# Performance work log

Measured on AMD Instinct MI355X. Metric: run time of the kernel, lower is better.

## Reference

```python
import jax, jax.numpy as jnp
import numpy as np

VOCAB, EMB, HDIM, VDIM, ATT = 30000, 256, 512, 128, 256
B, N, T = 64, 196, 32


def setup_inputs() -> dict:
    key = jax.random.key(0)
    ks = jax.random.split(key, 8)
    s = 0.02
    return {
        "V": jax.random.normal(ks[0], (B, N, VDIM), jnp.float32),
        "y": jax.random.randint(ks[1], (B, T), 0, VOCAB),
        "embed": jax.random.normal(ks[2], (VOCAB, EMB), jnp.float32) * s,
        "att_W_w": jax.random.normal(ks[3], (ATT, HDIM), jnp.float32) * s,
        "att_W_b": jnp.zeros((ATT,), jnp.float32),
        "att_U_w": jax.random.normal(ks[4], (ATT, VDIM), jnp.float32) * s,
        "att_U_b": jnp.zeros((ATT,), jnp.float32),
        "att_v_w": jax.random.normal(ks[5], (1, ATT), jnp.float32) * s,
        "att_v_b": jnp.zeros((1,), jnp.float32),
        "W_ih": jax.random.normal(ks[6], (4 * HDIM, EMB + VDIM), jnp.float32) * s,
        "W_hh": jax.random.normal(ks[7], (4 * HDIM, HDIM), jnp.float32) * s,
        "b_ih": jnp.zeros((4 * HDIM,), jnp.float32),
        "b_hh": jnp.zeros((4 * HDIM,), jnp.float32),
        "proj_w": jax.random.normal(jax.random.fold_in(key, 9), (EMB, HDIM), jnp.float32) * s,
    }


def reference(V, y, embed, att_W_w, att_W_b, att_U_w, att_U_b, att_v_w, att_v_b,
              W_ih, W_hh, b_ih, b_hh, proj_w):
    Bsz = y.shape[0]
    hdim = W_hh.shape[1]
    # loop-invariant U(V): [B, N, ATT]
    UV = jnp.einsum('bnv,av->bna', V, att_U_w) + att_U_b

    def step(carry, y_t):
        h, c, x_t = carry
        # additive attention
        Wh = h @ att_W_w.T + att_W_b                      # [B, ATT]
        e = jnp.tanh(Wh[:, None, :] + UV) @ att_v_w.T + att_v_b  # [B, N, 1]
        a = jax.nn.softmax(e, axis=1)
        ctx = jnp.sum(a * V, axis=1)                      # [B, VDIM]
        # LSTMCell (PyTorch gate order i, f, g, o)
        xc = jnp.concatenate([x_t, ctx], axis=-1)
        gates = xc @ W_ih.T + b_ih + h @ W_hh.T + b_hh
        i, f, g, o = jnp.split(gates, 4, axis=-1)
        c_new = jax.nn.sigmoid(f) * c + jax.nn.sigmoid(i) * jnp.tanh(g)
        h_new = jax.nn.sigmoid(o) * jnp.tanh(c_new)
        # dropout is identity in eval mode
        e_t = h_new @ proj_w.T                            # [B, EMB]
        logit = e_t @ embed.T                             # [B, VOCAB]
        x_next = embed[y_t]                               # teacher forcing
        return (h_new, c_new, x_next), logit

    h0 = jnp.zeros((Bsz, hdim), V.dtype)
    c0 = jnp.zeros((Bsz, hdim), V.dtype)
    x0 = embed[y[:, 0]]
    _, logits = jax.lax.scan(step, (h0, c0, x0), y[:, 1:].T)  # [T-1, B, VOCAB]
    return jnp.transpose(logits, (1, 0, 2))
```

## Files before the change

kernel.cpp:

```cpp
#include <hip/hip_runtime.h>
#include <stdint.h>

typedef unsigned short u16;
typedef uint32_t u32;
typedef short s16x8 __attribute__((ext_vector_type(8)));
typedef float f32x4 __attribute__((ext_vector_type(4)));

#define DEV __device__ __forceinline__

#define TSCALE 2.885390082f

DEV float bf2f(u16 h){ union{u32 u; float f;} x; x.u = ((u32)h)<<16; return x.f; }
DEV u16 f2bf(float f){ union{float f; u32 u;} x; x.f = f; u32 u = x.u;
  return (u16)((u + 0x7fffu + ((u>>16)&1u))>>16); }
DEV float bflo(u32 w){ union{u32 u; float f;} x; x.u = w<<16; return x.f; }
DEV float bfhi(u32 w){ union{u32 u; float f;} x; x.u = w & 0xffff0000u; return x.f; }

DEV float exp2_fast(float x){ return __builtin_amdgcn_exp2f(x); }
DEV float rcp_fast(float x){ return __builtin_amdgcn_rcpf(x); }
DEV float tanh2(float x){ float t = exp2_fast(TSCALE*x);
  return fmaf(-2.f, rcp_fast(t + 1.f), 1.f); }
DEV float sig2(float x){ return rcp_fast(1.f + exp2_fast(-1.442695041f*x)); }

DEV u32   ld_u(const u32* p){ return __hip_atomic_load(p, __ATOMIC_RELAXED, __HIP_MEMORY_SCOPE_AGENT); }
DEV void  st_u(u32* p, u32 v){ __hip_atomic_store(p, v, __ATOMIC_RELAXED, __HIP_MEMORY_SCOPE_AGENT); }

__global__ void f2b_kernel(const float* __restrict__ src, u16* __restrict__ dst, int n4, float scale){
  int i = blockIdx.x*blockDim.x + threadIdx.x;
  if (i < n4) {
    float4 v = ((const float4*)src)[i];
    ushort4 o; o.x = f2bf(v.x*scale); o.y = f2bf(v.y*scale); o.z = f2bf(v.z*scale); o.w = f2bf(v.w*scale);
    ((ushort4*)dst)[i] = o;
  }
}

__global__ void prep_wih2b(const float* __restrict__ Wih, u16* __restrict__ Wc){
  int idx = blockIdx.x*256 + threadIdx.x;
  int j = idx>>7, k = idx&127;
  Wc[idx] = f2bf(Wih[(size_t)j*384 + 256 + k]);
}

__global__ void repack_h(const u16* __restrict__ H2, u16* __restrict__ Hl){
  int r = blockIdx.x;
  int s = r>>6, b = r&63;
  int tid = threadIdx.x;
  u32 v = *((const u32*)(H2 + (size_t)(s+1)*32768 + (size_t)(tid>>2)*512 + (size_t)b*8) + (tid&3));
  ((u32*)(Hl + (size_t)r*512))[tid] = v;
}

__global__ __launch_bounds__(256) void gemm_bt(
    const u16* __restrict__ A, int lda,
    const u16* __restrict__ B, int ldb,
    const float* __restrict__ bias1, const float* __restrict__ bias2, float bscale,
    void* __restrict__ C, int ldc,
    int M, int N, int K, int Mt, int mode)
{
  __shared__ __align__(16) u16 As[64*64];
  __shared__ __align__(16) u16 Bs[128*64];
  int nwg = (int)gridDim.x;
  int b0 = blockIdx.x;
  int qq = nwg >> 3, rr = nwg & 7;
  int bswz;
  if (qq == 0) bswz = b0;
  else {
    int xcd = b0 & 7, i = b0 >> 3;
    bswz = (xcd < rr) ? (xcd*(qq+1) + i) : (rr*(qq+1) + (xcd - rr)*qq + i);
  }
  int mt = bswz % Mt, nt = bswz / Mt;
  int m0 = mt*64, n0 = nt*128;
  int tid = threadIdx.x, wave = tid>>6, lane = tid&63;
  int lrow = lane>>3, lcol = (lane&7)*8;
  f32x4 acc[2][4];
  #pragma unroll
  for (int i=0;i<2;i++)
    #pragma unroll
    for (int j=0;j<4;j++) acc[i][j] = (f32x4){0,0,0,0};
  int wm = (wave>>1)*32, wn = (wave&1)*64;
  int fr = lane&15, fk = (lane>>4)*8;
  for (int k0 = 0; k0 < K; k0 += 64) {
    __syncthreads();
    #pragma unroll
    for (int i = 0; i < 2; i++) {
      int ci = wave + i*4;
      int row = ci*8 + lrow;
      const u16* g = A + (size_t)(m0+row)*lda + k0 + lcol;
      __builtin_amdgcn_global_load_lds(
        (const __attribute__((address_space(1))) u32*)g,
        (__attribute__((address_space(3))) u32*)&As[ci*512], 16, 0, 0);
    }
    #pragma unroll
    for (int i = 0; i < 4; i++) {
      int ci = wave + i*4;
      int row = ci*8 + lrow;
      int gr = n0 + row; gr = gr < N ? gr : N-1;
      const u16* g = B + (size_t)gr*ldb + k0 + lcol;
      __builtin_amdgcn_global_load_lds(
        (const __attribute__((address_space(1))) u32*)g,
        (__attribute__((address_space(3))) u32*)&Bs[ci*512], 16, 0, 0);
    }
    __syncthreads();
    #pragma unroll
    for (int kk = 0; kk < 2; kk++) {
      s16x8 af[2], bfv[4];
      #pragma unroll
      for (int mi=0; mi<2; mi++)
        af[mi] = *(const s16x8*)&As[(wm + mi*16 + fr)*64 + kk*32 + fk];
      #pragma unroll
      for (int ni=0; ni<4; ni++)
        bfv[ni] = *(const s16x8*)&Bs[(wn + ni*16 + fr)*64 + kk*32 + fk];
      #pragma unroll
      for (int mi=0; mi<2; mi++)
        #pragma unroll
        for (int ni=0; ni<4; ni++)
          acc[mi][ni] = __builtin_amdgcn_mfma_f32_16x16x32_bf16(af[mi], bfv[ni], acc[mi][ni], 0,0,0);
    }
  }
  #pragma unroll
  for (int mi=0; mi<2; mi++)
    #pragma unroll
    for (int ni=0; ni<4; ni++) {
      int col = n0 + wn + ni*16 + (lane&15);
      if (col >= N) continue;
      float bv = 0.0f;
      if (bias1) bv += bias1[col];
      if (bias2) bv += bias2[col];
      bv *= bscale;
      int rbase = m0 + wm + mi*16 + ((lane>>4)<<2);
      #pragma unroll
      for (int r=0; r<4; r++) {
        int row = rbase + r;
        float v = acc[mi][ni][r] + bv;
        if (mode == 0) ((float*)C)[(size_t)row*ldc + col] = v;
        else if (mode == 1) ((u16*)C)[(size_t)row*ldc + col] = f2bf(v);
        else { int orow = (row&63)*31 + (row>>6); ((float*)C)[(size_t)orow*ldc + col] = v; }
      }
    }
}

__global__ void gather_x(const int* __restrict__ y, const float* __restrict__ embed, u16* __restrict__ X)
{
  int r = blockIdx.x;
  int s = r>>6, b = r&63;
  int tok = y[b*32 + s];
  X[(size_t)r*256 + threadIdx.x] = f2bf(embed[(size_t)tok*256 + threadIdx.x]);
}

#define NB 64

DEV void gbar(u32* flags, int bid, unsigned g){
  __asm__ volatile("" ::: "memory");
  __builtin_amdgcn_s_waitcnt(0);
  __syncthreads();
  if (threadIdx.x == 0) st_u(&flags[bid*16], g);
  if (threadIdx.x < 64) {
    for (;;) {
      u32 a = ld_u(&flags[threadIdx.x*16]);
      if (__all(a >= g)) break;
      __builtin_amdgcn_s_sleep(1);
    }
  }
  __syncthreads();
  __asm__ volatile("" ::: "memory");
}

__global__ __launch_bounds__(512, 1) void decoder_steps(
    const float* __restrict__ V,
    const float* __restrict__ attWb,
    const float* __restrict__ attvw,
    const float* __restrict__ attvb,
    const u16* __restrict__ WhhB,
    const u16* __restrict__ attWwB,
    const u16* __restrict__ WcB,
    u16* __restrict__ H2,
    const u16* __restrict__ UV,
    const u16* __restrict__ Xg,
    u16* __restrict__ CtxB,
    u32* __restrict__ flags)
{
  int bid = blockIdx.x, tid = threadIdx.x;
  int wave = tid>>6, lane = tid&63;
  int fr = lane&15, fkq = lane>>4;

  __shared__ __align__(16) u16 Wlds[32][648];
  __shared__ __align__(16) u16 Xglds[64][32];
  __shared__ float hls[512];
  __shared__ float whs[256];
  __shared__ float vws[256];
  __shared__ float esc[200];
  __shared__ float red1;
  __shared__ float part[512];

  {
    int r = tid>>4, p = tid&15;
    int grow = ((r>>3)<<9) + bid*8 + (r&7);
    #pragma unroll
    for (int i=0;i<5;i++){
      int k = p*40 + i*8;
      const u16* src = (k < 512) ? (WhhB + (size_t)grow*512 + k)
                                 : (WcB  + (size_t)grow*128 + (k-512));
      *(s16x8*)&Wlds[r][k] = *(const s16x8*)src;
    }
  }
  if (tid < 256) vws[tid] = attvw[tid];
  float vb = attvb[0];
  float c_reg[4] = {0.f,0.f,0.f,0.f};
  unsigned gen = 0;
  __syncthreads();

  int br = wave*16 + fr;

  for (int t = 0; t < 31; t++) {
    s16x8 af[16];
    s16x8 xg;
    if (tid < 256) {
      const u16* Hbase = H2 + (size_t)t*32768 + (size_t)br*8;
      #pragma unroll
      for (int kt=0;kt<16;kt++) af[kt] = *(const s16x8*)(Hbase + (size_t)(kt*4+fkq)*512);
    } else {
      int t2 = tid - 256;
      u32 hv = *((const u32*)(H2 + (size_t)t*32768 + (size_t)(t2>>2)*512 + (size_t)bid*8) + (t2&3));
      hls[2*t2]   = bflo(hv);
      hls[2*t2+1] = bfhi(hv);
      xg = *(const s16x8*)(Xg + (size_t)t*131072 + (size_t)(t2>>2)*2048 + (size_t)(t2&3)*512 + (size_t)bid*8);
    }
    __syncthreads();

    {
      int a_ = tid>>1, kh = (tid&1)*256;
      const u32* wr = (const u32*)(attWwB + (size_t)a_*512 + kh);
      float acc = (tid&1) ? 0.f : TSCALE * attWb[a_];
      #pragma unroll 4
      for (int k=0;k<256;k+=8){
        u32 w0 = wr[(k>>1)+0], w1 = wr[(k>>1)+1], w2 = wr[(k>>1)+2], w3 = wr[(k>>1)+3];
        float4 h0 = *(const float4*)&hls[kh+k];
        float4 h1 = *(const float4*)&hls[kh+k+4];
        acc = fmaf(bflo(w0), h0.x, acc); acc = fmaf(bfhi(w0), h0.y, acc);
        acc = fmaf(bflo(w1), h0.z, acc); acc = fmaf(bfhi(w1), h0.w, acc);
        acc = fmaf(bflo(w2), h1.x, acc); acc = fmaf(bfhi(w2), h1.y, acc);
        acc = fmaf(bflo(w3), h1.z, acc); acc = fmaf(bfhi(w3), h1.w, acc);
      }
      acc += __shfl_xor(acc, 1);
      if (!(tid&1)) whs[a_] = acc;
    }

    f32x4 a0 = (f32x4){0,0,0,0}, a1 = (f32x4){0,0,0,0};
    if (tid < 256) {
      #pragma unroll
      for (int kt=0;kt<16;kt++){
        s16x8 b0 = *(const s16x8*)&Wlds[fr][kt*32 + fkq*8];
        s16x8 b1 = *(const s16x8*)&Wlds[16+fr][kt*32 + fkq*8];
        a0 = __builtin_amdgcn_mfma_f32_16x16x32_bf16(af[kt], b0, a0, 0,0,0);
        a1 = __builtin_amdgcn_mfma_f32_16x16x32_bf16(af[kt], b1, a1, 0,0,0);
      }
      __builtin_amdgcn_sched_barrier(0);
    }
    __syncthreads();

    if (tid < 392) {
      int n = tid>>1, kh = (tid&1)*128;
      const u32* uvp = (const u32*)(UV + ((size_t)bid*196 + n)*256 + kh);
      float e0 = 0.0f, e1 = 0.0f;
      #pragma unroll 4
      for (int a = 0; a < 128; a += 4) {
        u32 uw0 = uvp[(a>>1)], uw1 = uvp[(a>>1)+1];
        float4 w4 = *(const float4*)&whs[kh+a];
        float4 v4 = *(const float4*)&vws[kh+a];
        float t0 = exp2_fast(w4.x + bflo(uw0));
        float t1 = exp2_fast(w4.y + bfhi(uw0));
        float t2 = exp2_fast(w4.z + bflo(uw1));
        float t3 = exp2_fast(w4.w + bfhi(uw1));
        e0 = fmaf(v4.x, fmaf(-2.f, rcp_fast(t0+1.f), 1.f), e0);
        e1 = fmaf(v4.y, fmaf(-2.f, rcp_fast(t1+1.f), 1.f), e1);
        e0 = fmaf(v4.z, fmaf(-2.f, rcp_fast(t2+1.f), 1.f), e0);
        e1 = fmaf(v4.w, fmaf(-2.f, rcp_fast(t3+1.f), 1.f), e1);
      }
      float e = e0 + e1;
      e += __shfl_xor(e, 1);
      if (!(tid&1)) esc[n] = exp2_fast(1.442695041f*(e + vb));
    }
    if (tid >= 256) {
      int t2 = tid - 256;
      *(s16x8*)&Xglds[t2>>2][(t2&3)*8] = xg;
    }
    __syncthreads();

    if (tid < 64) {
      float s = esc[tid] + esc[64+tid] + esc[128+tid];
      if (tid < 4)  s += esc[192+tid];
      #pragma unroll
      for (int off=32; off>=1; off>>=1) s += __shfl_xor(s, off);
      if (tid==0) red1 = s;
    }
    {
      int k = tid&127, q4 = tid>>7;
      const float* vp = V + ((size_t)bid*196 + q4*49)*128 + k;
      float a = 0.f;
      for (int n2=0; n2<49; n2++) a = fmaf(esc[q4*49+n2], vp[(size_t)n2*128], a);
      part[tid] = a;
    }
    __syncthreads();

    if (tid < 64) {
      float inv = rcp_fast(red1);
      float c0 = (part[2*tid]   + part[128+2*tid] + part[256+2*tid] + part[384+2*tid]) * inv;
      float c1 = (part[2*tid+1] + part[129+2*tid] + part[257+2*tid] + part[385+2*tid]) * inv;
      u32 pk = (u32)f2bf(c0) | ((u32)f2bf(c1) << 16);
      st_u((u32*)(CtxB + (size_t)t*8192 + (size_t)bid*128) + tid, pk);
    }
    gen++; gbar(flags, bid, gen);

    if (tid < 256) {
      const u16* Crow = CtxB + (size_t)t*8192 + (size_t)br*128 + fkq*8;
      #pragma unroll
      for (int kt=0;kt<4;kt++){
        s16x8 cf = *(const s16x8*)(Crow + kt*32);
        s16x8 b0 = *(const s16x8*)&Wlds[fr][(16+kt)*32 + fkq*8];
        s16x8 b1 = *(const s16x8*)&Wlds[16+fr][(16+kt)*32 + fkq*8];
        a0 = __builtin_amdgcn_mfma_f32_16x16x32_bf16(cf, b0, a0, 0,0,0);
        a1 = __builtin_amdgcn_mfma_f32_16x16x32_bf16(cf, b1, a1, 0,0,0);
      }
      int c = fr;
      int xr0 = ((c>>3)&1)*8 + (c&7);
      float v0[4], v1[4], s0[4], s1[4];
      #pragma unroll
      for (int r=0;r<4;r++){
        int b_r = wave*16 + fkq*4 + r;
        v0[r] = a0[r] + bf2f(Xglds[b_r][xr0]);
        v1[r] = a1[r] + bf2f(Xglds[b_r][16+xr0]);
      }
      #pragma unroll
      for (int r=0;r<4;r++){ s0[r] = __shfl_xor(v0[r], 8); s1[r] = __shfl_xor(v1[r], 8); }
      if (c < 8) {
        #pragma unroll
        for (int r=0;r<4;r++){
          int b_r = wave*16 + fkq*4 + r;
          float ig = sig2(v0[r]);
          float fg = sig2(s0[r]);
          float gg = tanh2(v1[r]);
          float og = sig2(s1[r]);
          float cn = fmaf(fg, c_reg[r], ig*gg);
          c_reg[r] = cn;
          float hvv = og * tanh2(cn);
          float hp = __shfl_xor(hvv, 1);
          if (!(c&1)) {
            u32 pk = (u32)f2bf(hvv) | ((u32)f2bf(hp) << 16);
            st_u((u32*)(H2 + (size_t)(t+1)*32768 + (size_t)bid*512 + (size_t)b_r*8) + (c>>1), pk);
          }
        }
      }
    }
    if (t < 30) { gen++; gbar(flags, bid, gen); }
  }
}

#define OFF_H    1024u
#define OFF_UV   2098176u
#define OFF_X    8520704u
#define OFF_XG   9536512u
#define OFF_GH   17662976u
#define OFF_EMB  OFF_GH
#define OFF_WH   33915904u
#define OFF_E    35947520u
#define OFF_VB   36963328u
#define OFF_WIH  40174592u
#define OFF_WHH  41747456u
#define OFF_AWW  43844608u
#define OFF_AUW  44106752u
#define OFF_PRJ  44172288u

extern "C" void kernel_launch(void* const* d_in, const int* in_sizes, int n_in,
                              void* d_out, int out_size, void* d_ws, size_t ws_size,
                              hipStream_t stream)
{
  const float* V      = (const float*)d_in[0];
  const int*   y      = (const int*)  d_in[1];
  const float* embed  = (const float*)d_in[2];
  const float* attWw  = (const float*)d_in[3];
  const float* attWb  = (const float*)d_in[4];
  const float* attUw  = (const float*)d_in[5];
  const float* attUb  = (const float*)d_in[6];
  const float* attvw  = (const float*)d_in[7];
  const float* attvb  = (const float*)d_in[8];
  const float* Wih    = (const float*)d_in[9];
  const float* Whh    = (const float*)d_in[10];
  const float* bih    = (const float*)d_in[11];
  const float* bhh    = (const float*)d_in[12];
  const float* projw  = (const float*)d_in[13];
  float* out = (float*)d_out;
  char* ws = (char*)d_ws;

  u16*   H2   = (u16*)  (ws + OFF_H);
  u16*   UVb  = (u16*)  (ws + OFF_UV);
  u16*   Xb   = (u16*)  (ws + OFF_X);
  u16*   Xg   = (u16*)  (ws + OFF_XG);
  u16*   Hl   = (u16*)  (ws + OFF_XG);
  u32*   flags= (u32*)  (ws + OFF_WH);
  u16*   CtxB = (u16*)  (ws + OFF_WH + 8192);
  u16*   E    = (u16*)  (ws + OFF_E);
  u16*   Vb   = (u16*)  (ws + OFF_VB);
  u16*   WcB  = (u16*)  (ws + OFF_VB);
  u16*   embB = (u16*)  (ws + OFF_EMB);
  u16*   WihB = (u16*)  (ws + OFF_WIH);
  u16*   WhhB = (u16*)  (ws + OFF_WHH);
  u16*   attWwB = (u16*)(ws + OFF_AWW);
  u16*   attUwB = (u16*)(ws + OFF_AUW);
  u16*   projB  = (u16*)(ws + OFF_PRJ);

  hipMemsetAsync(ws + OFF_H, 0, 65536, stream);
  hipMemsetAsync(ws + OFF_WH, 0, 4096, stream);

  f2b_kernel<<<(401408+255)/256, 256, 0, stream>>>(V,     Vb,     401408, 1.0f);
  f2b_kernel<<<(196608+255)/256, 256, 0, stream>>>(Wih,   WihB,   196608, 1.0f);
  f2b_kernel<<<(262144+255)/256, 256, 0, stream>>>(Whh,   WhhB,   262144, 1.0f);
  f2b_kernel<<<(32768+255)/256,  256, 0, stream>>>(attWw, attWwB,  32768, TSCALE);
  f2b_kernel<<<(8192+255)/256,   256, 0, stream>>>(attUw, attUwB,   8192, TSCALE);
  f2b_kernel<<<(32768+255)/256,  256, 0, stream>>>(projw, projB,   32768, 1.0f);
  f2b_kernel<<<(1920000+255)/256, 256, 0, stream>>>(embed, embB, 1920000, 1.0f);

  gather_x<<<1984, 256, 0, stream>>>(y, embed, Xb);

  gemm_bt<<<196*2, 256, 0, stream>>>(Vb, 128, attUwB, 128, attUb, nullptr, TSCALE,
                                     UVb, 256, 12544, 256, 128, 196, 1);
  prep_wih2b<<<1024, 256, 0, stream>>>(Wih, WcB);
  gemm_bt<<<31*16, 256, 0, stream>>>(Xb, 256, WihB, 384, bih, bhh, 1.0f,
                                     Xg, 2048, 1984, 2048, 256, 31, 1);

  decoder_steps<<<NB, 512, 0, stream>>>(V, attWb, attvw, attvb,
      WhhB, attWwB, WcB, H2, UVb, Xg, CtxB, flags);

  repack_h<<<1984, 256, 0, stream>>>(H2, Hl);

  gemm_bt<<<31*2, 256, 0, stream>>>(Hl, 512, projB, 512, nullptr, nullptr, 1.0f,
                                    E, 256, 1984, 256, 512, 31, 1);
  gemm_bt<<<31*235, 256, 0, stream>>>(E, 256, embB, 256, nullptr, nullptr, 1.0f,
                                      out, 30000, 1984, 30000, 256, 31, 2);
}
```

Before: 968.5 us.

## Fuse prep kernels, add 64x256 GEMM tile, reorder decoder h load

The seven f32-to-bf16 conversion launches and the embedding gather are merged into one block-partitioned prep kernel to cut launch overhead. A new GEMM variant with 64x256 tiles, XCD-aware block swizzling and direct global-to-LDS loads replaces the old GEMM for the UV, input-gate and large vocab logit products, aiming for better B-operand reuse and fewer blocks. In the decoder loop the h staging into LDS is split out with its own barrier before the fragment loads. The wider tiles reduce block count, which may lower occupancy and clamp padded rows on the last vocab tile.

```diff
diff --git a/kernel.cpp b/kernel.cpp
--- a/kernel.cpp
+++ b/kernel.cpp
@@ -25,12 +25,32 @@
 DEV u32   ld_u(const u32* p){ return __hip_atomic_load(p, __ATOMIC_RELAXED, __HIP_MEMORY_SCOPE_AGENT); }
 DEV void  st_u(u32* p, u32 v){ __hip_atomic_store(p, v, __ATOMIC_RELAXED, __HIP_MEMORY_SCOPE_AGENT); }
 
-__global__ void f2b_kernel(const float* __restrict__ src, u16* __restrict__ dst, int n4, float scale){
-  int i = blockIdx.x*blockDim.x + threadIdx.x;
-  if (i < n4) {
-    float4 v = ((const float4*)src)[i];
-    ushort4 o; o.x = f2bf(v.x*scale); o.y = f2bf(v.y*scale); o.z = f2bf(v.z*scale); o.w = f2bf(v.w*scale);
-    ((ushort4*)dst)[i] = o;
+DEV void cvt4(const float* __restrict__ src, u16* __restrict__ dst, int i, float scale){
+  float4 v = ((const float4*)src)[i];
+  ushort4 o; o.x = f2bf(v.x*scale); o.y = f2bf(v.y*scale); o.z = f2bf(v.z*scale); o.w = f2bf(v.w*scale);
+  ((ushort4*)dst)[i] = o;
+}
+__global__ void prep_all(
+    const float* __restrict__ V, const float* __restrict__ Wih, const float* __restrict__ Whh,
+    const float* __restrict__ attWw, const float* __restrict__ attUw, const float* __restrict__ projw,
+    const float* __restrict__ embed, const int* __restrict__ y,
+    u16* __restrict__ Vb, u16* __restrict__ WihB, u16* __restrict__ WhhB,
+    u16* __restrict__ attWwB, u16* __restrict__ attUwB, u16* __restrict__ projB,
+    u16* __restrict__ embB, u16* __restrict__ Xb)
+{
+  int blk = blockIdx.x, tid = threadIdx.x;
+  if      (blk < 1568)  cvt4(V,     Vb,     blk*256 + tid, 1.0f);
+  else if (blk < 2336)  cvt4(Wih,   WihB,   (blk-1568)*256 + tid, 1.0f);
+  else if (blk < 3360)  cvt4(Whh,   WhhB,   (blk-2336)*256 + tid, 1.0f);
+  else if (blk < 3488)  cvt4(attWw, attWwB, (blk-3360)*256 + tid, TSCALE);
+  else if (blk < 3520)  cvt4(attUw, attUwB, (blk-3488)*256 + tid, TSCALE);
+  else if (blk < 3648)  cvt4(projw, projB,  (blk-3520)*256 + tid, 1.0f);
+  else if (blk < 11148) cvt4(embed, embB,   (blk-3648)*256 + tid, 1.0f);
+  else {
+    int r = blk - 11148;
+    int s = r>>6, b = r&63;
+    int tok = y[b*32 + s];
+    Xb[(size_t)r*256 + tid] = f2bf(embed[(size_t)tok*256 + tid]);
   }
 }
 
@@ -137,12 +157,92 @@
     }
 }
 
-__global__ void gather_x(const int* __restrict__ y, const float* __restrict__ embed, u16* __restrict__ X)
+__global__ __launch_bounds__(256) void gemm_bt256(
+    const u16* __restrict__ A, int lda,
+    const u16* __restrict__ B, int ldb,
+    const float* __restrict__ bias1, const float* __restrict__ bias2, float bscale,
+    void* __restrict__ C, int ldc,
+    int M, int N, int K, int Mt, int mode)
 {
-  int r = blockIdx.x;
-  int s = r>>6, b = r&63;
-  int tok = y[b*32 + s];
-  X[(size_t)r*256 + threadIdx.x] = f2bf(embed[(size_t)tok*256 + threadIdx.x]);
+  __shared__ __align__(16) u16 As[64*64];
+  __shared__ __align__(16) u16 Bs[256*64];
+  int nwg = (int)gridDim.x;
+  int b0 = blockIdx.x;
+  int qq = nwg >> 3, rr = nwg & 7;
+  int bswz;
+  if (qq == 0) bswz = b0;
+  else {
+    int xcd = b0 & 7, i = b0 >> 3;
+    bswz = (xcd < rr) ? (xcd*(qq+1) + i) : (rr*(qq+1) + (xcd - rr)*qq + i);
+  }
+  int mt = bswz % Mt, nt = bswz / Mt;
+  int m0 = mt*64, n0 = nt*256;
+  int tid = threadIdx.x, wave = tid>>6, lane = tid&63;
+  int lrow = lane>>3, lcol = (lane&7)*8;
+  f32x4 acc[4][4];
+  #pragma unroll
+  for (int i=0;i<4;i++)
+    #pragma unroll
+    for (int j=0;j<4;j++) acc[i][j] = (f32x4){0,0,0,0};
+  int fr = lane&15, fk = (lane>>4)*8;
+  for (int k0 = 0; k0 < K; k0 += 64) {
+    __syncthreads();
+    #pragma unroll
+    for (int i = 0; i < 2; i++) {
+      int ci = wave*2 + i;
+      int row = ci*8 + lrow;
+      const u16* g = A + (size_t)(m0+row)*lda + k0 + lcol;
+      __builtin_amdgcn_global_load_lds(
+        (const __attribute__((address_space(1))) u32*)g,
+        (__attribute__((address_space(3))) u32*)&As[ci*512], 16, 0, 0);
+    }
+    #pragma unroll
+    for (int i = 0; i < 8; i++) {
+      int ci = wave*8 + i;
+      int row = ci*8 + lrow;
+      int gr = n0 + row; gr = gr < N ? gr : N-1;
+      const u16* g = B + (size_t)gr*ldb + k0 + lcol;
+      __builtin_amdgcn_global_load_lds(
+        (const __attribute__((address_space(1))) u32*)g,
+        (__attribute__((address_space(3))) u32*)&Bs[ci*512], 16, 0, 0);
+    }
+    __syncthreads();
+    #pragma unroll
+    for (int kk = 0; kk < 2; kk++) {
+      s16x8 af[4], bfv[4];
+      #pragma unroll
+      for (int mi=0; mi<4; mi++)
+        af[mi] = *(const s16x8*)&As[(mi*16 + fr)*64 + kk*32 + fk];
+      #pragma unroll
+      for (int ni=0; ni<4; ni++)
+        bfv[ni] = *(const s16x8*)&Bs[(wave*64 + ni*16 + fr)*64 + kk*32 + fk];
+      #pragma unroll
+      for (int mi=0; mi<4; mi++)
+        #pragma unroll
+        for (int ni=0; ni<4; ni++)
+          acc[mi][ni] = __builtin_amdgcn_mfma_f32_16x16x32_bf16(af[mi], bfv[ni], acc[mi][ni], 0,0,0);
+    }
+  }
+  #pragma unroll
+  for (int mi=0; mi<4; mi++)
+    #pragma unroll
+    for (int ni=0; ni<4; ni++) {
+      int col = n0 + wave*64 + ni*16 + (lane&15);
+      if (col >= N) continue;
+      float bv = 0.0f;
+      if (bias1) bv += bias1[col];
+      if (bias2) bv += bias2[col];
+      bv *= bscale;
+      int rbase = m0 + mi*16 + ((lane>>4)<<2);
+      #pragma unroll
+      for (int r=0; r<4; r++) {
+        int row = rbase + r;
+        float v = acc[mi][ni][r] + bv;
+        if (mode == 0) ((float*)C)[(size_t)row*ldc + col] = v;
+        else if (mode == 1) ((u16*)C)[(size_t)row*ldc + col] = f2bf(v);
+        else { int orow = (row&63)*31 + (row>>6); ((float*)C)[(size_t)orow*ldc + col] = v; }
+      }
+    }
 }
 
 #define NB 64
@@ -210,6 +310,14 @@
   int br = wave*16 + fr;
 
   for (int t = 0; t < 31; t++) {
+    if (tid >= 256) {
+      int t2 = tid - 256;
+      u32 hv = *((const u32*)(H2 + (size_t)t*32768 + (size_t)(t2>>2)*512 + (size_t)bid*8) + (t2&3));
+      hls[2*t2]   = bflo(hv);
+      hls[2*t2+1] = bfhi(hv);
+    }
+    __syncthreads();
+
     s16x8 af[16];
     s16x8 xg;
     if (tid < 256) {
@@ -218,12 +326,8 @@
       for (int kt=0;kt<16;kt++) af[kt] = *(const s16x8*)(Hbase + (size_t)(kt*4+fkq)*512);
     } else {
       int t2 = tid - 256;
-      u32 hv = *((const u32*)(H2 + (size_t)t*32768 + (size_t)(t2>>2)*512 + (size_t)bid*8) + (t2&3));
-      hls[2*t2]   = bflo(hv);
-      hls[2*t2+1] = bfhi(hv);
       xg = *(const s16x8*)(Xg + (size_t)t*131072 + (size_t)(t2>>2)*2048 + (size_t)(t2&3)*512 + (size_t)bid*8);
     }
-    __syncthreads();
 
     {
       int a_ = tid>>1, kh = (tid&1)*256;
@@ -409,21 +513,14 @@
   hipMemsetAsync(ws + OFF_H, 0, 65536, stream);
   hipMemsetAsync(ws + OFF_WH, 0, 4096, stream);
 
-  f2b_kernel<<<(401408+255)/256, 256, 0, stream>>>(V,     Vb,     401408, 1.0f);
-  f2b_kernel<<<(196608+255)/256, 256, 0, stream>>>(Wih,   WihB,   196608, 1.0f);
-  f2b_kernel<<<(262144+255)/256, 256, 0, stream>>>(Whh,   WhhB,   262144, 1.0f);
-  f2b_kernel<<<(32768+255)/256,  256, 0, stream>>>(attWw, attWwB,  32768, TSCALE);
-  f2b_kernel<<<(8192+255)/256,   256, 0, stream>>>(attUw, attUwB,   8192, TSCALE);
-  f2b_kernel<<<(32768+255)/256,  256, 0, stream>>>(projw, projB,   32768, 1.0f);
-  f2b_kernel<<<(1920000+255)/256, 256, 0, stream>>>(embed, embB, 1920000, 1.0f);
-
-  gather_x<<<1984, 256, 0, stream>>>(y, embed, Xb);
-
-  gemm_bt<<<196*2, 256, 0, stream>>>(Vb, 128, attUwB, 128, attUb, nullptr, TSCALE,
-                                     UVb, 256, 12544, 256, 128, 196, 1);
+  prep_all<<<13132, 256, 0, stream>>>(V, Wih, Whh, attWw, attUw, projw, embed, y,
+                                      Vb, WihB, WhhB, attWwB, attUwB, projB, embB, Xb);
+
+  gemm_bt256<<<196, 256, 0, stream>>>(Vb, 128, attUwB, 128, attUb, nullptr, TSCALE,
+                                      UVb, 256, 12544, 256, 128, 196, 1);
   prep_wih2b<<<1024, 256, 0, stream>>>(Wih, WcB);
-  gemm_bt<<<31*16, 256, 0, stream>>>(Xb, 256, WihB, 384, bih, bhh, 1.0f,
-                                     Xg, 2048, 1984, 2048, 256, 31, 1);
+  gemm_bt256<<<31*8, 256, 0, stream>>>(Xb, 256, WihB, 384, bih, bhh, 1.0f,
+                                       Xg, 2048, 1984, 2048, 256, 31, 1);
 
   decoder_steps<<<NB, 512, 0, stream>>>(V, attWb, attvw, attvb,
       WhhB, attWwB, WcB, H2, UVb, Xg, CtxB, flags);
@@ -432,6 +529,6 @@
 
   gemm_bt<<<31*2, 256, 0, stream>>>(Hl, 512, projB, 512, nullptr, nullptr, 1.0f,
                                     E, 256, 1984, 256, 512, 31, 1);
-  gemm_bt<<<31*235, 256, 0, stream>>>(E, 256, embB, 256, nullptr, nullptr, 1.0f,
-                                      out, 30000, 1984, 30000, 256, 31, 2);
-}
+  gemm_bt256<<<31*118, 256, 0, stream>>>(E, 256, embB, 256, nullptr, nullptr, 1.0f,
+                                         out, 30000, 1984, 30000, 256, 31, 2);
+}
```

Result: slower. 1.007 ms (+4.0%).
